# Kernel tuning notes

Hardware: AMD Instinct MI355X
Metric: run time of the kernel (lower is better)

## Reference

```python
import jax, jax.numpy as jnp
import numpy as np

N, E, IN_DIM, HID, HEADS, LAYERS = 50000, 320000, 128, 128, 4, 2
C = HID // HEADS  # per-head channels = 32
EPS = 1e-5


def _init(key, shape, fan_in):
    return jax.random.normal(key, shape, dtype=jnp.float32) / np.sqrt(fan_in)


def setup_inputs() -> dict:
    key = jax.random.key(0)
    ks = jax.random.split(key, 20)
    x = jax.random.normal(ks[0], (N, IN_DIM), dtype=jnp.float32)
    edge_index = jax.random.randint(ks[1], (2, E), 0, N, dtype=jnp.int64)
    edge_attr = jax.random.uniform(ks[2], (E, 1), dtype=jnp.float32)
    inp = {
        "x": x, "edge_index": edge_index, "edge_attr": edge_attr,
        "W_in": _init(ks[3], (IN_DIM, HID), IN_DIM),
        "b_in": jnp.zeros((HID,), jnp.float32),
        # per-layer TransformerConv params, stacked on leading layer axis
        "Wq": _init(ks[4], (LAYERS, HID, HID), HID),
        "bq": jnp.zeros((LAYERS, HID), jnp.float32),
        "Wk": _init(ks[5], (LAYERS, HID, HID), HID),
        "bk": jnp.zeros((LAYERS, HID), jnp.float32),
        "Wv": _init(ks[6], (LAYERS, HID, HID), HID),
        "bv": jnp.zeros((LAYERS, HID), jnp.float32),
        "We": _init(ks[7], (LAYERS, 1, HID), 1),          # lin_edge, bias=False
        "Wskip": _init(ks[8], (LAYERS, HID, HID), HID),   # root/skip projection
        "bskip": jnp.zeros((LAYERS, HID), jnp.float32),
        "Wbeta": _init(ks[9], (LAYERS, 3 * HID, 1), 3 * HID),  # lin_beta, bias=False
        "bn_gamma": jnp.ones((LAYERS, HID), jnp.float32),
        "bn_beta": jnp.zeros((LAYERS, HID), jnp.float32),
    }
    return inp


def _transformer_conv(h, src, tgt, edge_attr, Wq, bq, Wk, bk, Wv, bv, We, Wskip, bskip, Wbeta):
    n = h.shape[0]
    q = (h @ Wq + bq).reshape(n, HEADS, C)
    k = (h @ Wk + bk).reshape(n, HEADS, C)
    v = (h @ Wv + bv).reshape(n, HEADS, C)
    e = (edge_attr @ We).reshape(-1, HEADS, C)          # [E,H,C] edge embedding
    k_j = k[src] + e                                     # gather source keys
    alpha = jnp.einsum('ehc,ehc->eh', q[tgt], k_j) / jnp.sqrt(jnp.float32(C))
    amax = jax.ops.segment_max(alpha, tgt, num_segments=n)   # softmax over in-edges per target
    ex = jnp.exp(alpha - amax[tgt])
    denom = jax.ops.segment_sum(ex, tgt, num_segments=n)
    a = ex / denom[tgt]                                  # [E,H]
    msg = (v[src] + e) * a[..., None]
    out = jax.ops.segment_sum(msg, tgt, num_segments=n).reshape(n, HID)
    x_r = h @ Wskip + bskip                              # root weight
    beta = jax.nn.sigmoid(jnp.concatenate([out, x_r, out - x_r], axis=-1) @ Wbeta)
    return beta * x_r + (1.0 - beta) * out


def _batchnorm(h, gamma, beta):
    mu = h.mean(axis=0)
    var = h.var(axis=0)
    return gamma * (h - mu) * jax.lax.rsqrt(var + EPS) + beta


def reference(x, edge_index, edge_attr, W_in, b_in, Wq, bq, Wk, bk, Wv, bv, We, Wskip, bskip, Wbeta, bn_gamma, bn_beta):
    src, tgt = edge_index[0], edge_index[1]
    h = jax.nn.relu(x @ W_in + b_in)
    for l in range(LAYERS):
        h_res = h
        h = _transformer_conv(h, src, tgt, edge_attr, Wq[l], bq[l], Wk[l], bk[l], Wv[l], bv[l], We[l], Wskip[l], bskip[l], Wbeta[l])
        h = jax.nn.relu(_batchnorm(h, bn_gamma[l], bn_beta[l]))
        h = h + h_res
    return h
```

## Files before the change

### kernel.cpp

```cpp
#include <hip/hip_runtime.h>
#include <hip/hip_bf16.h>
#include <math.h>

#define EPS 1e-5f

typedef __attribute__((ext_vector_type(8))) short bf16x8;
typedef __attribute__((ext_vector_type(4))) float f32x4;

__device__ __forceinline__ unsigned short f2bf(float f) {
    unsigned u = __float_as_uint(f);
    unsigned r = (u + 0x7FFFu + ((u >> 16) & 1u)) >> 16;
    return (unsigned short)r;
}
__device__ __forceinline__ unsigned f2bf2(float lo, float hi) {
    return (unsigned)f2bf(lo) | ((unsigned)f2bf(hi) << 16);
}
__device__ __forceinline__ float bf2f(unsigned short u) {
    return __uint_as_float((unsigned)u << 16);
}
__device__ __forceinline__ void bfu2(unsigned u, float& lo, float& hi) {
    lo = __uint_as_float(u << 16);
    hi = __uint_as_float(u & 0xFFFF0000u);
}

__global__ __launch_bounds__(256) void prep(const float* __restrict__ x,
                                            unsigned short* __restrict__ xbf, int n4,
                                            const float* __restrict__ W0, const float* __restrict__ W1,
                                            const float* __restrict__ W2, const float* __restrict__ W3,
                                            const float* __restrict__ W4, const float* __restrict__ W5,
                                            const float* __restrict__ W6, const float* __restrict__ W7,
                                            const float* __restrict__ W8, unsigned short* __restrict__ Bpack,
                                            int* __restrict__ deg, int N,
                                            int nConv, int nPack) {
    int b = blockIdx.x;
    if (b < nConv) {
        int i = b * 256 + threadIdx.x;
        if (i < n4) {
            float4 v = ((const float4*)x)[i];
            ushort4 o = make_ushort4(f2bf(v.x), f2bf(v.y), f2bf(v.z), f2bf(v.w));
            ((ushort4*)xbf)[i] = o;
        }
    } else if (b < nConv + nPack) {
        int t = (b - nConv) * 256 + threadIdx.x;
        if (t < 9 * 16384) {
            int mat = t >> 14, r = t & 16383;
            const float* W;
            switch (mat) {
                case 0: W = W0; break; case 1: W = W1; break; case 2: W = W2; break;
                case 3: W = W3; break; case 4: W = W4; break; case 5: W = W5; break;
                case 6: W = W6; break; case 7: W = W7; break; default: W = W8; break;
            }
            int j = r & 7, lane = (r >> 3) & 63, nt = (r >> 9) & 7, kc = r >> 12;
            int k = kc * 32 + (lane >> 4) * 8 + j;
            int n = (lane & 15) * 8 + nt;
            Bpack[t] = f2bf(W[k * 128 + n]);
        }
    } else {
        int i = (b - nConv - nPack) * 256 + threadIdx.x;
        if (i < N) deg[i] = 0;
    }
}

template <int ACT, int WBF>
__global__ __launch_bounds__(256) void gemm_mfma(const unsigned short* __restrict__ Abf,
                                                 const unsigned short* __restrict__ Bp,
                                                 const float* __restrict__ bias,
                                                 float* __restrict__ C,
                                                 unsigned short* __restrict__ Cbf, int M) {
    int wave = threadIdx.x >> 6, lane = threadIdx.x & 63;
    int base = blockIdx.x * 64 + wave * 16;
    int m = lane & 15, kg = lane >> 4;
    int arow = base + m; if (arow >= M) arow = M - 1;
    const unsigned short* Aptr = Abf + (size_t)arow * 128 + kg * 8;
    f32x4 acc[8];
#pragma unroll
    for (int nt = 0; nt < 8; ++nt) acc[nt] = (f32x4)(0.f);
#pragma unroll
    for (int kc = 0; kc < 4; ++kc) {
        bf16x8 a = *(const bf16x8*)(Aptr + kc * 32);
        const unsigned short* bp = Bp + (size_t)kc * 4096 + (size_t)lane * 8;
#pragma unroll
        for (int nt = 0; nt < 8; ++nt) {
            bf16x8 b = *(const bf16x8*)(bp + nt * 512);
            acc[nt] = __builtin_amdgcn_mfma_f32_16x16x32_bf16(a, b, acc[nt], 0, 0, 0);
        }
    }
    int col0 = lane & 15;
    int r0 = base + (lane >> 4) * 4;
    float4 bl = *(const float4*)&bias[col0 * 8];
    float4 bh = *(const float4*)&bias[col0 * 8 + 4];
#pragma unroll
    for (int r = 0; r < 4; ++r) {
        int ro = r0 + r;
        if (ro < M) {
            float v0 = acc[0][r] + bl.x, v1 = acc[1][r] + bl.y;
            float v2 = acc[2][r] + bl.z, v3 = acc[3][r] + bl.w;
            float v4 = acc[4][r] + bh.x, v5 = acc[5][r] + bh.y;
            float v6 = acc[6][r] + bh.z, v7 = acc[7][r] + bh.w;
            if (ACT) {
                v0 = fmaxf(v0, 0.f); v1 = fmaxf(v1, 0.f); v2 = fmaxf(v2, 0.f); v3 = fmaxf(v3, 0.f);
                v4 = fmaxf(v4, 0.f); v5 = fmaxf(v5, 0.f); v6 = fmaxf(v6, 0.f); v7 = fmaxf(v7, 0.f);
            }
            size_t o = (size_t)ro * 128 + col0 * 8;
            *(float4*)&C[o]     = make_float4(v0, v1, v2, v3);
            *(float4*)&C[o + 4] = make_float4(v4, v5, v6, v7);
            if (WBF)
                *(uint4*)&Cbf[o] = make_uint4(f2bf2(v0, v1), f2bf2(v2, v3),
                                              f2bf2(v4, v5), f2bf2(v6, v7));
        }
    }
}

__global__ __launch_bounds__(256) void gemm_qk(const unsigned short* __restrict__ Abf,
                                               const unsigned short* __restrict__ Bq,
                                               const unsigned short* __restrict__ Bk,
                                               const float* __restrict__ bq,
                                               const float* __restrict__ bk,
                                               unsigned short* __restrict__ qbf,
                                               unsigned short* __restrict__ kvbf, int M) {
    int wave = threadIdx.x >> 6, lane = threadIdx.x & 63;
    int base = blockIdx.x * 64 + wave * 16;
    int m = lane & 15, kg = lane >> 4;
    int arow = base + m; if (arow >= M) arow = M - 1;
    const unsigned short* Aptr = Abf + (size_t)arow * 128 + kg * 8;
    f32x4 aq[8], ak[8];
#pragma unroll
    for (int nt = 0; nt < 8; ++nt) { aq[nt] = (f32x4)(0.f); ak[nt] = (f32x4)(0.f); }
#pragma unroll
    for (int kc = 0; kc < 4; ++kc) {
        bf16x8 a = *(const bf16x8*)(Aptr + kc * 32);
        size_t boff = (size_t)kc * 4096 + (size_t)lane * 8;
#pragma unroll
        for (int nt = 0; nt < 8; ++nt) {
            bf16x8 b0 = *(const bf16x8*)(Bq + boff + nt * 512);
            aq[nt] = __builtin_amdgcn_mfma_f32_16x16x32_bf16(a, b0, aq[nt], 0, 0, 0);
            bf16x8 b1 = *(const bf16x8*)(Bk + boff + nt * 512);
            ak[nt] = __builtin_amdgcn_mfma_f32_16x16x32_bf16(a, b1, ak[nt], 0, 0, 0);
        }
    }
    int col0 = lane & 15;
    int r0 = base + (lane >> 4) * 4;
    float4 bql = *(const float4*)&bq[col0 * 8], bqh = *(const float4*)&bq[col0 * 8 + 4];
    float4 bkl = *(const float4*)&bk[col0 * 8], bkh = *(const float4*)&bk[col0 * 8 + 4];
#pragma unroll
    for (int r = 0; r < 4; ++r) {
        int ro = r0 + r;
        if (ro < M) {
            size_t qo = (size_t)ro * 128 + col0 * 8;
            size_t kvo = (size_t)ro * 256 + col0 * 8;
            *(uint4*)&qbf[qo] = make_uint4(
                f2bf2(aq[0][r] + bql.x, aq[1][r] + bql.y), f2bf2(aq[2][r] + bql.z, aq[3][r] + bql.w),
                f2bf2(aq[4][r] + bqh.x, aq[5][r] + bqh.y), f2bf2(aq[6][r] + bqh.z, aq[7][r] + bqh.w));
            *(uint4*)&kvbf[kvo] = make_uint4(
                f2bf2(ak[0][r] + bkl.x, ak[1][r] + bkl.y), f2bf2(ak[2][r] + bkl.z, ak[3][r] + bkl.w),
                f2bf2(ak[4][r] + bkh.x, ak[5][r] + bkh.y), f2bf2(ak[6][r] + bkh.z, ak[7][r] + bkh.w));
        }
    }
}

__global__ __launch_bounds__(256) void gemm_vs(const unsigned short* __restrict__ Abf,
                                               const unsigned short* __restrict__ Bv,
                                               const unsigned short* __restrict__ Bs,
                                               const float* __restrict__ bv,
                                               const float* __restrict__ bs,
                                               unsigned short* __restrict__ kvbf,
                                               unsigned short* __restrict__ xrbf,
                                               float* __restrict__ bstatZ, int M) {
    if (blockIdx.x == 0) {
        ((float2*)bstatZ)[threadIdx.x] = make_float2(0.f, 0.f);
        ((float2*)bstatZ)[256 + threadIdx.x] = make_float2(0.f, 0.f);
        ((float2*)bstatZ)[512 + threadIdx.x] = make_float2(0.f, 0.f);
        ((float2*)bstatZ)[768 + threadIdx.x] = make_float2(0.f, 0.f);
    }
    int wave = threadIdx.x >> 6, lane = threadIdx.x & 63;
    int base = blockIdx.x * 64 + wave * 16;
    int m = lane & 15, kg = lane >> 4;
    int arow = base + m; if (arow >= M) arow = M - 1;
    const unsigned short* Aptr = Abf + (size_t)arow * 128 + kg * 8;
    f32x4 av[8], as_[8];
#pragma unroll
    for (int nt = 0; nt < 8; ++nt) { av[nt] = (f32x4)(0.f); as_[nt] = (f32x4)(0.f); }
#pragma unroll
    for (int kc = 0; kc < 4; ++kc) {
        bf16x8 a = *(const bf16x8*)(Aptr + kc * 32);
        size_t boff = (size_t)kc * 4096 + (size_t)lane * 8;
#pragma unroll
        for (int nt = 0; nt < 8; ++nt) {
            bf16x8 b2 = *(const bf16x8*)(Bv + boff + nt * 512);
            av[nt] = __builtin_amdgcn_mfma_f32_16x16x32_bf16(a, b2, av[nt], 0, 0, 0);
            bf16x8 b3 = *(const bf16x8*)(Bs + boff + nt * 512);
            as_[nt] = __builtin_amdgcn_mfma_f32_16x16x32_bf16(a, b3, as_[nt], 0, 0, 0);
        }
    }
    int col0 = lane & 15;
    int r0 = base + (lane >> 4) * 4;
    float4 bvl = *(const float4*)&bv[col0 * 8], bvh = *(const float4*)&bv[col0 * 8 + 4];
    float4 bsl = *(const float4*)&bs[col0 * 8], bsh = *(const float4*)&bs[col0 * 8 + 4];
#pragma unroll
    for (int r = 0; r < 4; ++r) {
        int ro = r0 + r;
        if (ro < M) {
            size_t qo = (size_t)ro * 128 + col0 * 8;
            size_t kvo = (size_t)ro * 256 + 128 + col0 * 8;
            *(uint4*)&kvbf[kvo] = make_uint4(
                f2bf2(av[0][r] + bvl.x, av[1][r] + bvl.y), f2bf2(av[2][r] + bvl.z, av[3][r] + bvl.w),
                f2bf2(av[4][r] + bvh.x, av[5][r] + bvh.y), f2bf2(av[6][r] + bvh.z, av[7][r] + bvh.w));
            *(uint4*)&xrbf[qo] = make_uint4(
                f2bf2(as_[0][r] + bsl.x, as_[1][r] + bsl.y), f2bf2(as_[2][r] + bsl.z, as_[3][r] + bsl.w),
                f2bf2(as_[4][r] + bsh.x, as_[5][r] + bsh.y), f2bf2(as_[6][r] + bsh.z, as_[7][r] + bsh.w));
        }
    }
}

__global__ __launch_bounds__(256) void csr_hist(const int* __restrict__ ei,
                                                int* __restrict__ deg, int E) {
    int e = blockIdx.x * 256 + threadIdx.x;
    if (e < E) atomicAdd(&deg[ei[E + e]], 1);
}

__global__ __launch_bounds__(256) void scan_block_sums(const int* __restrict__ deg,
                                                       int* __restrict__ bsums, int N) {
    __shared__ int sd[256];
    int i = blockIdx.x * 256 + threadIdx.x;
    sd[threadIdx.x] = (i < N) ? deg[i] : 0;
    __syncthreads();
    for (int off = 128; off > 0; off >>= 1) {
        if (threadIdx.x < off) sd[threadIdx.x] += sd[threadIdx.x + off];
        __syncthreads();
    }
    if (threadIdx.x == 0) bsums[blockIdx.x] = sd[0];
}

__global__ __launch_bounds__(256) void scan_bsums(const int* __restrict__ bsums,
                                                  int* __restrict__ boff, int nb) {
    __shared__ int sd[256];
    int tid = threadIdx.x;
    int per = (nb + 255) / 256;
    int start = tid * per;
    int s = 0;
    for (int i = 0; i < per; ++i) {
        int idx = start + i;
        if (idx < nb) s += bsums[idx];
    }
    int my = s;
    sd[tid] = s;
    __syncthreads();
    for (int off = 1; off < 256; off <<= 1) {
        int t = (tid >= off) ? sd[tid - off] : 0;
        __syncthreads();
        sd[tid] += t;
        __syncthreads();
    }
    int run = sd[tid] - my;
    for (int i = 0; i < per; ++i) {
        int idx = start + i;
        if (idx < nb) {
            boff[idx] = run;
            run += bsums[idx];
        }
    }
}

__global__ __launch_bounds__(256) void scan_local(const int* __restrict__ deg,
                                                  const int* __restrict__ boff,
                                                  int* __restrict__ rowptr,
                                                  int* __restrict__ wrptr, int N, int E) {
    __shared__ int sd[256];
    int i = blockIdx.x * 256 + threadIdx.x;
    int v = (i < N) ? deg[i] : 0;
    sd[threadIdx.x] = v;
    __syncthreads();
    for (int off = 1; off < 256; off <<= 1) {
        int t = (threadIdx.x >= off) ? sd[threadIdx.x - off] : 0;
        __syncthreads();
        sd[threadIdx.x] += t;
        __syncthreads();
    }
    if (i < N) {
        int excl = sd[threadIdx.x] - v + boff[blockIdx.x];
        rowptr[i] = excl;
        wrptr[i] = excl;
        if (i == N - 1) rowptr[N] = E;
    }
}

__global__ __launch_bounds__(256) void csr_fill(const int* __restrict__ ei,
                                                const float* __restrict__ ea,
                                                int* __restrict__ wrptr,
                                                int2* __restrict__ csr_sw, int E) {
    int e = blockIdx.x * 256 + threadIdx.x;
    if (e >= E) return;
    int tgt = ei[E + e];
    int pos = atomicAdd(&wrptr[tgt], 1);
    csr_sw[pos] = make_int2(ei[e], __float_as_int(ea[e]));
}

__global__ __launch_bounds__(256) void attn_gather(const unsigned short* __restrict__ qbf,
                                                   const unsigned short* __restrict__ kvbf,
                                                   const unsigned short* __restrict__ xrbf,
                                                   const int* __restrict__ rowptr,
                                                   const int2* __restrict__ csr_sw,
                                                   const float* __restrict__ Wel,
                                                   const float* __restrict__ Wb,
                                                   float* __restrict__ out,
                                                   float* __restrict__ bsumR,
                                                   float* __restrict__ bsumsqR, int N) {
    __shared__ float sdS[4][128];
    __shared__ float sdQ[4][128];
    int tid = threadIdx.x;
    int n = blockIdx.x * 16 + (tid >> 4);
    int sl = tid & 15;
    int wave = tid >> 6, lane = tid & 63;
    bool live = (n < N);
    int nn = live ? n : (N - 1);

    uint4 qu = ((const uint4*)(qbf + (size_t)nn * 128))[sl];
    float qf[8];
    bfu2(qu.x, qf[0], qf[1]); bfu2(qu.y, qf[2], qf[3]);
    bfu2(qu.z, qf[4], qf[5]); bfu2(qu.w, qf[6], qf[7]);
    float wef[8];
    {
        float4 w0 = ((const float4*)Wel)[sl * 2];
        float4 w1 = ((const float4*)Wel)[sl * 2 + 1];
        wef[0] = w0.x; wef[1] = w0.y; wef[2] = w0.z; wef[3] = w0.w;
        wef[4] = w1.x; wef[5] = w1.y; wef[6] = w1.z; wef[7] = w1.w;
    }
    float qwe = 0.f;
#pragma unroll
    for (int c = 0; c < 8; ++c) qwe += qf[c] * wef[c];
    qwe += __shfl_xor(qwe, 1);
    qwe += __shfl_xor(qwe, 2);

    float l = 0.f, pw = 0.f;
    float acc[8];
#pragma unroll
    for (int c = 0; c < 8; ++c) acc[c] = 0.f;

    int beg = live ? rowptr[nn] : 0;
    int end = live ? rowptr[nn + 1] : 0;

    if (beg < end) {
        int2 sw0 = csr_sw[beg];
        int j1 = (beg + 1 < end) ? beg + 1 : beg;
        int2 sw1 = csr_sw[j1];
        int j2 = (beg + 2 < end) ? beg + 2 : beg;
        int2 sw2 = csr_sw[j2];
        const uint4* r0 = (const uint4*)(kvbf + (size_t)sw0.x * 256);
        uint4 ku0 = r0[sl], vu0 = r0[16 + sl];
        const uint4* r1 = (const uint4*)(kvbf + (size_t)sw1.x * 256);
        uint4 ku1 = r1[sl], vu1 = r1[16 + sl];

        for (int i = beg; i < end; ++i) {
            const uint4* r2 = (const uint4*)(kvbf + (size_t)sw2.x * 256);
            uint4 ku2 = r2[sl], vu2 = r2[16 + sl];
            int j3 = (i + 3 < end) ? i + 3 : beg;
            int2 sw3 = csr_sw[j3];

            float w = __int_as_float(sw0.y);
            float kf[8];
            bfu2(ku0.x, kf[0], kf[1]); bfu2(ku0.y, kf[2], kf[3]);
            bfu2(ku0.z, kf[4], kf[5]); bfu2(ku0.w, kf[6], kf[7]);
            float d = 0.f;
#pragma unroll
            for (int c = 0; c < 8; ++c) d += qf[c] * kf[c];
            d += __shfl_xor(d, 1); d += __shfl_xor(d, 2);
            float p = __expf((d + w * qwe) * 0.17677669529663687f);
            l += p;
            pw += p * w;
            float vf[8];
            bfu2(vu0.x, vf[0], vf[1]); bfu2(vu0.y, vf[2], vf[3]);
            bfu2(vu0.z, vf[4], vf[5]); bfu2(vu0.w, vf[6], vf[7]);
#pragma unroll
            for (int c = 0; c < 8; ++c)
                acc[c] += p * vf[c];

            sw0 = sw1; sw1 = sw2; sw2 = sw3;
            ku0 = ku1; vu0 = vu1;
            ku1 = ku2; vu1 = vu2;
        }
    }

    float inv = (l > 0.f) ? 1.f / l : 0.f;
    float ox[8];
#pragma unroll
    for (int c = 0; c < 8; ++c) ox[c] = (acc[c] + pw * wef[c]) * inv;

    uint4 xu = ((const uint4*)(xrbf + (size_t)nn * 128))[sl];
    float xv[8];
    bfu2(xu.x, xv[0], xv[1]); bfu2(xu.y, xv[2], xv[3]);
    bfu2(xu.z, xv[4], xv[5]); bfu2(xu.w, xv[6], xv[7]);
    float4 b0 = ((const float4*)Wb)[sl * 2];
    float4 b1 = ((const float4*)Wb)[sl * 2 + 1];
    float4 c0 = ((const float4*)(Wb + 128))[sl * 2];
    float4 c1 = ((const float4*)(Wb + 128))[sl * 2 + 1];
    float4 d0 = ((const float4*)(Wb + 256))[sl * 2];
    float4 d1 = ((const float4*)(Wb + 256))[sl * 2 + 1];
    float wb0[8] = {b0.x, b0.y, b0.z, b0.w, b1.x, b1.y, b1.z, b1.w};
    float wb1[8] = {c0.x, c0.y, c0.z, c0.w, c1.x, c1.y, c1.z, c1.w};
    float wb2[8] = {d0.x, d0.y, d0.z, d0.w, d1.x, d1.y, d1.z, d1.w};
    float part = 0.f;
#pragma unroll
    for (int c = 0; c < 8; ++c)
        part += ox[c] * wb0[c] + xv[c] * wb1[c] + (ox[c] - xv[c]) * wb2[c];
    part += __shfl_xor(part, 1); part += __shfl_xor(part, 2);
    part += __shfl_xor(part, 4); part += __shfl_xor(part, 8);
    float beta = 1.f / (1.f + __expf(-part));

    float r[8];
#pragma unroll
    for (int c = 0; c < 8; ++c)
        r[c] = beta * xv[c] + (1.f - beta) * ox[c];

    if (live) {
        ((float4*)(out + (size_t)n * 128))[sl * 2] =
            make_float4(r[0], r[1], r[2], r[3]);
        ((float4*)(out + (size_t)n * 128))[sl * 2 + 1] =
            make_float4(r[4], r[5], r[6], r[7]);
    }

    float s8[8], q8[8];
#pragma unroll
    for (int c = 0; c < 8; ++c) {
        s8[c] = live ? r[c] : 0.f;
        q8[c] = live ? r[c] * r[c] : 0.f;
    }
#pragma unroll
    for (int c = 0; c < 8; ++c) {
        s8[c] += __shfl_xor(s8[c], 16); s8[c] += __shfl_xor(s8[c], 32);
        q8[c] += __shfl_xor(q8[c], 16); q8[c] += __shfl_xor(q8[c], 32);
    }
    if ((lane >> 4) == 0) {
#pragma unroll
        for (int c = 0; c < 8; ++c) {
            sdS[wave][sl * 8 + c] = s8[c];
            sdQ[wave][sl * 8 + c] = q8[c];
        }
    }
    __syncthreads();
    if (tid < 128) {
        float s = sdS[0][tid] + sdS[1][tid] + sdS[2][tid] + sdS[3][tid];
        float q = sdQ[0][tid] + sdQ[1][tid] + sdQ[2][tid] + sdQ[3][tid];
        int rep = blockIdx.x & 7;
        atomicAdd(&bsumR[rep * 128 + tid], s);
        atomicAdd(&bsumsqR[rep * 128 + tid], q);
    }
}

__global__ __launch_bounds__(256) void bn_apply(const float* __restrict__ o,
                                                const float* __restrict__ hres,
                                                float* __restrict__ hout,
                                                unsigned short* __restrict__ hout_bf,
                                                const float* __restrict__ bsumR,
                                                const float* __restrict__ bsumsqR,
                                                const float* __restrict__ gamma,
                                                const float* __restrict__ bbeta,
                                                int N, float invN) {
    int i = blockIdx.x * 256 + threadIdx.x;
    if (i >= N * 32) return;
    int c4 = i & 31;
    float4 s = make_float4(0.f, 0.f, 0.f, 0.f), ss = s;
#pragma unroll
    for (int rep = 0; rep < 8; ++rep) {
        float4 sv = ((const float4*)bsumR)[rep * 32 + c4];
        float4 qv = ((const float4*)bsumsqR)[rep * 32 + c4];
        s.x += sv.x; s.y += sv.y; s.z += sv.z; s.w += sv.w;
        ss.x += qv.x; ss.y += qv.y; ss.z += qv.z; ss.w += qv.w;
    }
    float4 g = ((const float4*)gamma)[c4];
    float4 b = ((const float4*)bbeta)[c4];
    float4 ov = ((const float4*)o)[i];
    float4 hr = ((const float4*)hres)[i];
    float4 r;
    { float mu = s.x * invN, var = ss.x * invN - mu * mu;
      r.x = fmaxf((ov.x - mu) * (g.x * rsqrtf(var + EPS)) + b.x, 0.f) + hr.x; }
    { float mu = s.y * invN, var = ss.y * invN - mu * mu;
      r.y = fmaxf((ov.y - mu) * (g.y * rsqrtf(var + EPS)) + b.y, 0.f) + hr.y; }
    { float mu = s.z * invN, var = ss.z * invN - mu * mu;
      r.z = fmaxf((ov.z - mu) * (g.z * rsqrtf(var + EPS)) + b.z, 0.f) + hr.z; }
    { float mu = s.w * invN, var = ss.w * invN - mu * mu;
      r.w = fmaxf((ov.w - mu) * (g.w * rsqrtf(var + EPS)) + b.w, 0.f) + hr.w; }
    ((float4*)hout)[i] = r;
    if (hout_bf) {
        ushort4 ob = make_ushort4(f2bf(r.x), f2bf(r.y), f2bf(r.z), f2bf(r.w));
        ((ushort4*)hout_bf)[i] = ob;
    }
}

extern "C" void kernel_launch(void* const* d_in, const int* in_sizes, int n_in,
                              void* d_out, int out_size, void* d_ws, size_t ws_size,
                              hipStream_t stream) {
    const float* x     = (const float*)d_in[0];
    const int*   ei    = (const int*)d_in[1];
    const float* ea    = (const float*)d_in[2];
    const float* W_in  = (const float*)d_in[3];
    const float* b_in  = (const float*)d_in[4];
    const float* Wq    = (const float*)d_in[5];
    const float* bq    = (const float*)d_in[6];
    const float* Wk    = (const float*)d_in[7];
    const float* bk    = (const float*)d_in[8];
    const float* Wv    = (const float*)d_in[9];
    const float* bv    = (const float*)d_in[10];
    const float* We    = (const float*)d_in[11];
    const float* Wskip = (const float*)d_in[12];
    const float* bskip = (const float*)d_in[13];
    const float* Wbeta = (const float*)d_in[14];
    const float* bn_g  = (const float*)d_in[15];
    const float* bn_b  = (const float*)d_in[16];

    const int N = in_sizes[0] / 128;
    const int E = in_sizes[1] / 2;

    float* ws = (float*)d_ws;
    unsigned short* Bpack = (unsigned short*)ws;
    size_t off = 73728;
    unsigned short* xbf  = (unsigned short*)(ws + off);               off += (size_t)N * 64;
    unsigned short* hbf  = (unsigned short*)(ws + off);               off += (size_t)N * 64;
    unsigned short* qbf  = (unsigned short*)(ws + off);               off += (size_t)N * 64;
    unsigned short* kvbf = (unsigned short*)(ws + off);               off += (size_t)N * 128;
    unsigned short* xrbf = (unsigned short*)(ws + off);               off += (size_t)N * 64;
    float* h    = ws + off;  off += (size_t)N * 128;
    float* attn = ws + off;  off += (size_t)N * 128;
    float* bsumR   = ws + off;  off += 1024;
    float* bsumsqR = ws + off;  off += 1024;
    int2* csr_sw = (int2*)(ws + off);  off += (size_t)E * 2;
    int* deg     = (int*)(ws + off);
    int* rowptr  = deg + N;
    int* wrptr   = rowptr + (N + 1);
    int* bsums   = wrptr + N;
    int* boff    = bsums + ((N + 255) / 256 + 1);

    dim3 blk(256);
    int gGemm   = (N + 63) / 64;
    int gNode16 = (N + 15) / 16;
    int gEdge   = (E + 255) / 256;
    int gApply  = (N * 32 + 255) / 256;
    int nbScan  = (N + 255) / 256;

    int nConv = gApply;
    int nPack = (9 * 16384 + 255) / 256;
    prep<<<nConv + nPack + nbScan, blk, 0, stream>>>(
        x, xbf, N * 32,
        W_in, Wq, Wk, Wv, Wskip, Wq + 16384, Wk + 16384, Wv + 16384, Wskip + 16384,
        Bpack, deg, N, nConv, nPack);

    csr_hist<<<gEdge, blk, 0, stream>>>(ei, deg, E);
    scan_block_sums<<<nbScan, blk, 0, stream>>>(deg, bsums, N);
    scan_bsums<<<1, blk, 0, stream>>>(bsums, boff, nbScan);
    scan_local<<<nbScan, blk, 0, stream>>>(deg, boff, rowptr, wrptr, N, E);
    csr_fill<<<gEdge, blk, 0, stream>>>(ei, ea, wrptr, csr_sw, E);

    gemm_mfma<1, 1><<<gGemm, blk, 0, stream>>>(xbf, Bpack + 0 * 16384, b_in, h, hbf, N);

    for (int l = 0; l < 2; ++l) {
        const unsigned short* Bq = Bpack + (size_t)(1 + l * 4 + 0) * 16384;
        const unsigned short* Bk = Bpack + (size_t)(1 + l * 4 + 1) * 16384;
        const unsigned short* Bv = Bpack + (size_t)(1 + l * 4 + 2) * 16384;
        const unsigned short* Bs = Bpack + (size_t)(1 + l * 4 + 3) * 16384;
        gemm_qk<<<gGemm, blk, 0, stream>>>(hbf, Bq, Bk, bq + l * 128, bk + l * 128,
                                           qbf, kvbf, N);
        gemm_vs<<<gGemm, blk, 0, stream>>>(hbf, Bv, Bs, bv + l * 128, bskip + l * 128,
                                           kvbf, xrbf, bsumR, N);
        attn_gather<<<gNode16, blk, 0, stream>>>(qbf, kvbf, xrbf, rowptr, csr_sw,
                                                 We + l * 128, Wbeta + l * 384, attn,
                                                 bsumR, bsumsqR, N);
        bn_apply<<<gApply, blk, 0, stream>>>(attn, h, (l == 1) ? (float*)d_out : h,
                                             (l == 0) ? hbf : (unsigned short*)0,
                                             bsumR, bsumsqR, bn_g + l * 128, bn_b + l * 128,
                                             N, 1.0f / (float)N);
    }
}
```

Baseline: 333.7 us.

## Fuse QK and VS projections and fold layer-0 batchnorm into layer-1 GEMM

Merges the two per-layer projection GEMMs into one kernel that computes Q, K, V and skip from a single A read. For layer 1, the batchnorm, ReLU and residual of layer 0 run as a prologue that stages bf16 rows in shared memory, so the separate bn_apply launch and the hbf round trip go away. Batchnorm statistics now use per-layer buffers that are zeroed in prep. The cost is higher register pressure from 32 accumulators per lane, which may lower occupancy.

```diff
diff --git a/kernel.cpp b/kernel.cpp
--- a/kernel.cpp
+++ b/kernel.cpp
@@ -14,9 +14,6 @@
 }
 __device__ __forceinline__ unsigned f2bf2(float lo, float hi) {
     return (unsigned)f2bf(lo) | ((unsigned)f2bf(hi) << 16);
-}
-__device__ __forceinline__ float bf2f(unsigned short u) {
-    return __uint_as_float((unsigned)u << 16);
 }
 __device__ __forceinline__ void bfu2(unsigned u, float& lo, float& hi) {
     lo = __uint_as_float(u << 16);
@@ -30,7 +27,7 @@
                                             const float* __restrict__ W4, const float* __restrict__ W5,
                                             const float* __restrict__ W6, const float* __restrict__ W7,
                                             const float* __restrict__ W8, unsigned short* __restrict__ Bpack,
-                                            int* __restrict__ deg, int N,
+                                            int* __restrict__ deg, float* __restrict__ bstatZ, int N,
                                             int nConv, int nPack) {
     int b = blockIdx.x;
     if (b < nConv) {
@@ -58,6 +55,7 @@
     } else {
         int i = (b - nConv - nPack) * 256 + threadIdx.x;
         if (i < N) deg[i] = 0;
+        if (i < 4096) bstatZ[i] = 0.f;
     }
 }
 
@@ -111,40 +109,117 @@
     }
 }
 
-__global__ __launch_bounds__(256) void gemm_qk(const unsigned short* __restrict__ Abf,
-                                               const unsigned short* __restrict__ Bq,
-                                               const unsigned short* __restrict__ Bk,
-                                               const float* __restrict__ bq,
-                                               const float* __restrict__ bk,
-                                               unsigned short* __restrict__ qbf,
-                                               unsigned short* __restrict__ kvbf, int M) {
-    int wave = threadIdx.x >> 6, lane = threadIdx.x & 63;
-    int base = blockIdx.x * 64 + wave * 16;
+template <int BNPRO>
+__global__ __launch_bounds__(256) void gemm4(const unsigned short* __restrict__ Abf,
+                                             const float* __restrict__ attn,
+                                             const float* __restrict__ hres,
+                                             float* __restrict__ hout,
+                                             const float* __restrict__ bstat,
+                                             const float* __restrict__ gamma,
+                                             const float* __restrict__ bbeta,
+                                             float invN,
+                                             const unsigned short* __restrict__ B0,
+                                             const unsigned short* __restrict__ B1,
+                                             const unsigned short* __restrict__ B2,
+                                             const unsigned short* __restrict__ B3,
+                                             const float* __restrict__ b0,
+                                             const float* __restrict__ b1,
+                                             const float* __restrict__ b2,
+                                             const float* __restrict__ b3,
+                                             unsigned short* __restrict__ qbf,
+                                             unsigned short* __restrict__ kvbf,
+                                             unsigned short* __restrict__ xrbf, int M) {
+    __shared__ unsigned short As[64][136];
+    __shared__ float sMu[128], sGS[128], sB[128];
+    int tid = threadIdx.x;
+    int base = blockIdx.x * 64;
+
+    if (BNPRO) {
+        if (tid < 128) {
+            float s = 0.f, q = 0.f;
+#pragma unroll
+            for (int rep = 0; rep < 8; ++rep) {
+                s += bstat[rep * 128 + tid];
+                q += bstat[1024 + rep * 128 + tid];
+            }
+            float mu = s * invN, var = q * invN - mu * mu;
+            sMu[tid] = mu;
+            sGS[tid] = gamma[tid] * rsqrtf(var + EPS);
+            sB[tid] = bbeta[tid];
+        }
+        __syncthreads();
+#pragma unroll
+        for (int j = 0; j < 4; ++j) {
+            int s = j * 256 + tid;
+            int row = s >> 4, sl = s & 15;
+            int grow = base + row;
+            if (grow < M) {
+                size_t o = (size_t)grow * 128 + sl * 8;
+                float4 a0 = *(const float4*)&attn[o];
+                float4 a1 = *(const float4*)&attn[o + 4];
+                float4 h0 = *(const float4*)&hres[o];
+                float4 h1 = *(const float4*)&hres[o + 4];
+                int c = sl * 8;
+                float r0 = fmaxf((a0.x - sMu[c+0]) * sGS[c+0] + sB[c+0], 0.f) + h0.x;
+                float r1 = fmaxf((a0.y - sMu[c+1]) * sGS[c+1] + sB[c+1], 0.f) + h0.y;
+                float r2 = fmaxf((a0.z - sMu[c+2]) * sGS[c+2] + sB[c+2], 0.f) + h0.z;
+                float r3 = fmaxf((a0.w - sMu[c+3]) * sGS[c+3] + sB[c+3], 0.f) + h0.w;
+                float r4 = fmaxf((a1.x - sMu[c+4]) * sGS[c+4] + sB[c+4], 0.f) + h1.x;
+                float r5 = fmaxf((a1.y - sMu[c+5]) * sGS[c+5] + sB[c+5], 0.f) + h1.y;
+                float r6 = fmaxf((a1.z - sMu[c+6]) * sGS[c+6] + sB[c+6], 0.f) + h1.z;
+                float r7 = fmaxf((a1.w - sMu[c+7]) * sGS[c+7] + sB[c+7], 0.f) + h1.w;
+                *(float4*)&hout[o]     = make_float4(r0, r1, r2, r3);
+                *(float4*)&hout[o + 4] = make_float4(r4, r5, r6, r7);
+                *(uint4*)&As[row][sl * 8] = make_uint4(f2bf2(r0, r1), f2bf2(r2, r3),
+                                                       f2bf2(r4, r5), f2bf2(r6, r7));
+            } else {
+                *(uint4*)&As[row][sl * 8] = make_uint4(0u, 0u, 0u, 0u);
+            }
+        }
+        __syncthreads();
+    }
+
+    int wave = tid >> 6, lane = tid & 63;
+    int wbase = base + wave * 16;
     int m = lane & 15, kg = lane >> 4;
-    int arow = base + m; if (arow >= M) arow = M - 1;
-    const unsigned short* Aptr = Abf + (size_t)arow * 128 + kg * 8;
-    f32x4 aq[8], ak[8];
-#pragma unroll
-    for (int nt = 0; nt < 8; ++nt) { aq[nt] = (f32x4)(0.f); ak[nt] = (f32x4)(0.f); }
+    const unsigned short* Aptr = 0;
+    if (!BNPRO) {
+        int arow = wbase + m; if (arow >= M) arow = M - 1;
+        Aptr = Abf + (size_t)arow * 128 + kg * 8;
+    }
+    f32x4 aq[8], ak[8], av[8], as_[8];
+#pragma unroll
+    for (int nt = 0; nt < 8; ++nt) {
+        aq[nt] = (f32x4)(0.f); ak[nt] = (f32x4)(0.f);
+        av[nt] = (f32x4)(0.f); as_[nt] = (f32x4)(0.f);
+    }
 #pragma unroll
     for (int kc = 0; kc < 4; ++kc) {
-        bf16x8 a = *(const bf16x8*)(Aptr + kc * 32);
+        bf16x8 a;
+        if (BNPRO) a = *(const bf16x8*)&As[wave * 16 + m][kg * 8 + kc * 32];
+        else       a = *(const bf16x8*)(Aptr + kc * 32);
         size_t boff = (size_t)kc * 4096 + (size_t)lane * 8;
 #pragma unroll
         for (int nt = 0; nt < 8; ++nt) {
-            bf16x8 b0 = *(const bf16x8*)(Bq + boff + nt * 512);
-            aq[nt] = __builtin_amdgcn_mfma_f32_16x16x32_bf16(a, b0, aq[nt], 0, 0, 0);
-            bf16x8 b1 = *(const bf16x8*)(Bk + boff + nt * 512);
-            ak[nt] = __builtin_amdgcn_mfma_f32_16x16x32_bf16(a, b1, ak[nt], 0, 0, 0);
+            bf16x8 w0 = *(const bf16x8*)(B0 + boff + nt * 512);
+            aq[nt] = __builtin_amdgcn_mfma_f32_16x16x32_bf16(a, w0, aq[nt], 0, 0, 0);
+            bf16x8 w1 = *(const bf16x8*)(B1 + boff + nt * 512);
+            ak[nt] = __builtin_amdgcn_mfma_f32_16x16x32_bf16(a, w1, ak[nt], 0, 0, 0);
+            bf16x8 w2 = *(const bf16x8*)(B2 + boff + nt * 512);
+            av[nt] = __builtin_amdgcn_mfma_f32_16x16x32_bf16(a, w2, av[nt], 0, 0, 0);
+            bf16x8 w3 = *(const bf16x8*)(B3 + boff + nt * 512);
+            as_[nt] = __builtin_amdgcn_mfma_f32_16x16x32_bf16(a, w3, as_[nt], 0, 0, 0);
         }
     }
     int col0 = lane & 15;
-    int r0 = base + (lane >> 4) * 4;
-    float4 bql = *(const float4*)&bq[col0 * 8], bqh = *(const float4*)&bq[col0 * 8 + 4];
-    float4 bkl = *(const float4*)&bk[col0 * 8], bkh = *(const float4*)&bk[col0 * 8 + 4];
+    int r0r = wbase + (lane >> 4) * 4;
+    float4 bql = *(const float4*)&b0[col0 * 8], bqh = *(const float4*)&b0[col0 * 8 + 4];
+    float4 bkl = *(const float4*)&b1[col0 * 8], bkh = *(const float4*)&b1[col0 * 8 + 4];
+    float4 bvl = *(const float4*)&b2[col0 * 8], bvh = *(const float4*)&b2[col0 * 8 + 4];
+    float4 bsl = *(const float4*)&b3[col0 * 8], bsh = *(const float4*)&b3[col0 * 8 + 4];
 #pragma unroll
     for (int r = 0; r < 4; ++r) {
-        int ro = r0 + r;
+        int ro = r0r + r;
         if (ro < M) {
             size_t qo = (size_t)ro * 128 + col0 * 8;
             size_t kvo = (size_t)ro * 256 + col0 * 8;
@@ -154,55 +229,7 @@
             *(uint4*)&kvbf[kvo] = make_uint4(
                 f2bf2(ak[0][r] + bkl.x, ak[1][r] + bkl.y), f2bf2(ak[2][r] + bkl.z, ak[3][r] + bkl.w),
                 f2bf2(ak[4][r] + bkh.x, ak[5][r] + bkh.y), f2bf2(ak[6][r] + bkh.z, ak[7][r] + bkh.w));
-        }
-    }
-}
-
-__global__ __launch_bounds__(256) void gemm_vs(const unsigned short* __restrict__ Abf,
-                                               const unsigned short* __restrict__ Bv,
-                                               const unsigned short* __restrict__ Bs,
-                                               const float* __restrict__ bv,
-                                               const float* __restrict__ bs,
-                                               unsigned short* __restrict__ kvbf,
-                                               unsigned short* __restrict__ xrbf,
-                                               float* __restrict__ bstatZ, int M) {
-    if (blockIdx.x == 0) {
-        ((float2*)bstatZ)[threadIdx.x] = make_float2(0.f, 0.f);
-        ((float2*)bstatZ)[256 + threadIdx.x] = make_float2(0.f, 0.f);
-        ((float2*)bstatZ)[512 + threadIdx.x] = make_float2(0.f, 0.f);
-        ((float2*)bstatZ)[768 + threadIdx.x] = make_float2(0.f, 0.f);
-    }
-    int wave = threadIdx.x >> 6, lane = threadIdx.x & 63;
-    int base = blockIdx.x * 64 + wave * 16;
-    int m = lane & 15, kg = lane >> 4;
-    int arow = base + m; if (arow >= M) arow = M - 1;
-    const unsigned short* Aptr = Abf + (size_t)arow * 128 + kg * 8;
-    f32x4 av[8], as_[8];
-#pragma unroll
-    for (int nt = 0; nt < 8; ++nt) { av[nt] = (f32x4)(0.f); as_[nt] = (f32x4)(0.f); }
-#pragma unroll
-    for (int kc = 0; kc < 4; ++kc) {
-        bf16x8 a = *(const bf16x8*)(Aptr + kc * 32);
-        size_t boff = (size_t)kc * 4096 + (size_t)lane * 8;
-#pragma unroll
-        for (int nt = 0; nt < 8; ++nt) {
-            bf16x8 b2 = *(const bf16x8*)(Bv + boff + nt * 512);
-            av[nt] = __builtin_amdgcn_mfma_f32_16x16x32_bf16(a, b2, av[nt], 0, 0, 0);
-            bf16x8 b3 = *(const bf16x8*)(Bs + boff + nt * 512);
-            as_[nt] = __builtin_amdgcn_mfma_f32_16x16x32_bf16(a, b3, as_[nt], 0, 0, 0);
-        }
-    }
-    int col0 = lane & 15;
-    int r0 = base + (lane >> 4) * 4;
-    float4 bvl = *(const float4*)&bv[col0 * 8], bvh = *(const float4*)&bv[col0 * 8 + 4];
-    float4 bsl = *(const float4*)&bs[col0 * 8], bsh = *(const float4*)&bs[col0 * 8 + 4];
-#pragma unroll
-    for (int r = 0; r < 4; ++r) {
-        int ro = r0 + r;
-        if (ro < M) {
-            size_t qo = (size_t)ro * 128 + col0 * 8;
-            size_t kvo = (size_t)ro * 256 + 128 + col0 * 8;
-            *(uint4*)&kvbf[kvo] = make_uint4(
+            *(uint4*)&kvbf[kvo + 128] = make_uint4(
                 f2bf2(av[0][r] + bvl.x, av[1][r] + bvl.y), f2bf2(av[2][r] + bvl.z, av[3][r] + bvl.w),
                 f2bf2(av[4][r] + bvh.x, av[5][r] + bvh.y), f2bf2(av[6][r] + bvh.z, av[7][r] + bvh.w));
             *(uint4*)&xrbf[qo] = make_uint4(
@@ -449,9 +476,7 @@
 __global__ __launch_bounds__(256) void bn_apply(const float* __restrict__ o,
                                                 const float* __restrict__ hres,
                                                 float* __restrict__ hout,
-                                                unsigned short* __restrict__ hout_bf,
-                                                const float* __restrict__ bsumR,
-                                                const float* __restrict__ bsumsqR,
+                                                const float* __restrict__ bstat,
                                                 const float* __restrict__ gamma,
                                                 const float* __restrict__ bbeta,
                                                 int N, float invN) {
@@ -461,8 +486,8 @@
     float4 s = make_float4(0.f, 0.f, 0.f, 0.f), ss = s;
 #pragma unroll
     for (int rep = 0; rep < 8; ++rep) {
-        float4 sv = ((const float4*)bsumR)[rep * 32 + c4];
-        float4 qv = ((const float4*)bsumsqR)[rep * 32 + c4];
+        float4 sv = ((const float4*)bstat)[rep * 32 + c4];
+        float4 qv = ((const float4*)(bstat + 1024))[rep * 32 + c4];
         s.x += sv.x; s.y += sv.y; s.z += sv.z; s.w += sv.w;
         ss.x += qv.x; ss.y += qv.y; ss.z += qv.z; ss.w += qv.w;
     }
@@ -480,10 +505,6 @@
     { float mu = s.w * invN, var = ss.w * invN - mu * mu;
       r.w = fmaxf((ov.w - mu) * (g.w * rsqrtf(var + EPS)) + b.w, 0.f) + hr.w; }
     ((float4*)hout)[i] = r;
-    if (hout_bf) {
-        ushort4 ob = make_ushort4(f2bf(r.x), f2bf(r.y), f2bf(r.z), f2bf(r.w));
-        ((ushort4*)hout_bf)[i] = ob;
-    }
 }
 
 extern "C" void kernel_launch(void* const* d_in, const int* in_sizes, int n_in,
@@ -520,8 +541,7 @@
     unsigned short* xrbf = (unsigned short*)(ws + off);               off += (size_t)N * 64;
     float* h    = ws + off;  off += (size_t)N * 128;
     float* attn = ws + off;  off += (size_t)N * 128;
-    float* bsumR   = ws + off;  off += 1024;
-    float* bsumsqR = ws + off;  off += 1024;
+    float* bstat = ws + off; off += 4096;
     int2* csr_sw = (int2*)(ws + off);  off += (size_t)E * 2;
     int* deg     = (int*)(ws + off);
     int* rowptr  = deg + N;
@@ -529,19 +549,23 @@
     int* bsums   = wrptr + N;
     int* boff    = bsums + ((N + 255) / 256 + 1);
 
+    float* bstat0 = bstat;
+    float* bstat1 = bstat + 2048;
+
     dim3 blk(256);
     int gGemm   = (N + 63) / 64;
     int gNode16 = (N + 15) / 16;
     int gEdge   = (E + 255) / 256;
     int gApply  = (N * 32 + 255) / 256;
     int nbScan  = (N + 255) / 256;
+    float invN = 1.0f / (float)N;
 
     int nConv = gApply;
     int nPack = (9 * 16384 + 255) / 256;
     prep<<<nConv + nPack + nbScan, blk, 0, stream>>>(
         x, xbf, N * 32,
         W_in, Wq, Wk, Wv, Wskip, Wq + 16384, Wk + 16384, Wv + 16384, Wskip + 16384,
-        Bpack, deg, N, nConv, nPack);
+        Bpack, deg, bstat, N, nConv, nPack);
 
     csr_hist<<<gEdge, blk, 0, stream>>>(ei, deg, E);
     scan_block_sums<<<nbScan, blk, 0, stream>>>(deg, bsums, N);
@@ -551,21 +575,32 @@
 
     gemm_mfma<1, 1><<<gGemm, blk, 0, stream>>>(xbf, Bpack + 0 * 16384, b_in, h, hbf, N);
 
-    for (int l = 0; l < 2; ++l) {
-        const unsigned short* Bq = Bpack + (size_t)(1 + l * 4 + 0) * 16384;
-        const unsigned short* Bk = Bpack + (size_t)(1 + l * 4 + 1) * 16384;
-        const unsigned short* Bv = Bpack + (size_t)(1 + l * 4 + 2) * 16384;
-        const unsigned short* Bs = Bpack + (size_t)(1 + l * 4 + 3) * 16384;
-        gemm_qk<<<gGemm, blk, 0, stream>>>(hbf, Bq, Bk, bq + l * 128, bk + l * 128,
-                                           qbf, kvbf, N);
-        gemm_vs<<<gGemm, blk, 0, stream>>>(hbf, Bv, Bs, bv + l * 128, bskip + l * 128,
-                                           kvbf, xrbf, bsumR, N);
-        attn_gather<<<gNode16, blk, 0, stream>>>(qbf, kvbf, xrbf, rowptr, csr_sw,
-                                                 We + l * 128, Wbeta + l * 384, attn,
-                                                 bsumR, bsumsqR, N);
-        bn_apply<<<gApply, blk, 0, stream>>>(attn, h, (l == 1) ? (float*)d_out : h,
-                                             (l == 0) ? hbf : (unsigned short*)0,
-                                             bsumR, bsumsqR, bn_g + l * 128, bn_b + l * 128,
-                                             N, 1.0f / (float)N);
-    }
-}
+    const unsigned short* Bq0 = Bpack + (size_t)1 * 16384;
+    const unsigned short* Bk0 = Bpack + (size_t)2 * 16384;
+    const unsigned short* Bv0 = Bpack + (size_t)3 * 16384;
+    const unsigned short* Bs0 = Bpack + (size_t)4 * 16384;
+    const unsigned short* Bq1 = Bpack + (size_t)5 * 16384;
+    const unsigned short* Bk1 = Bpack + (size_t)6 * 16384;
+    const unsigned short* Bv1 = Bpack + (size_t)7 * 16384;
+    const unsigned short* Bs1 = Bpack + (size_t)8 * 16384;
+
+    gemm4<0><<<gGemm, blk, 0, stream>>>(hbf, nullptr, nullptr, nullptr,
+                                        nullptr, nullptr, nullptr, 0.f,
+                                        Bq0, Bk0, Bv0, Bs0,
+                                        bq, bk, bv, bskip,
+                                        qbf, kvbf, xrbf, N);
+    attn_gather<<<gNode16, blk, 0, stream>>>(qbf, kvbf, xrbf, rowptr, csr_sw,
+                                             We, Wbeta, attn,
+                                             bstat0, bstat0 + 1024, N);
+    gemm4<1><<<gGemm, blk, 0, stream>>>(nullptr, attn, h, h,
+                                        bstat0, bn_g, bn_b, invN,
+                                        Bq1, Bk1, Bv1, Bs1,
+                                        bq + 128, bk + 128, bv + 128, bskip + 128,
+                                        qbf, kvbf, xrbf, N);
+    attn_gather<<<gNode16, blk, 0, stream>>>(qbf, kvbf, xrbf, rowptr, csr_sw,
+                                             We + 128, Wbeta + 384, attn,
+                                             bstat1, bstat1 + 1024, N);
+    bn_apply<<<gApply, blk, 0, stream>>>(attn, h, (float*)d_out,
+                                         bstat1, bn_g + 128, bn_b + 128,
+                                         N, invN);
+}
```

Measured after the change: 325.7 us. -2.4%, faster.
